# Performance work log

Measured on AMD Instinct MI355X. Metric: run time of the kernel, lower is better.

The kernel has to match this reference:

```python
import jax, jax.numpy as jnp
import numpy as np


def setup_inputs() -> dict:
    key = jax.random.key(0)
    k1, k2, k3, k4 = jax.random.split(key, 4)
    b, h, w = 16, 28, 28
    C = 3072  # 1024 + 2048
    L1 = 9    # num_landmarks + 1
    K = 2000  # num_classes
    l3 = jax.random.normal(k1, (b, 1024, h, w), dtype=jnp.float32)
    l4 = jax.random.normal(k2, (b, 2048, h // 2, w // 2), dtype=jnp.float32)
    W_land = jax.random.normal(k3, (L1, C), dtype=jnp.float32) * 0.02  # 1x1 conv weight
    W_class = jax.random.normal(k4, (K, C), dtype=jnp.float32) * 0.02
    modulation = jnp.ones((1, C, L1), dtype=jnp.float32)
    return {"l3": l3, "l4": l4, "W_land": W_land, "W_class": W_class, "modulation": modulation}


def reference(l3, l4, W_land, W_class, modulation):
    b, c3, h, w = l3.shape
    # bilinear upsample layer4 to layer3 spatial size (align_corners=False semantics)
    l4_up = jax.image.resize(l4, (l4.shape[0], l4.shape[1], h, w), method="bilinear")
    x = jnp.concatenate([l4_up, l3], axis=1)  # (b, 3072, h, w)

    ab = jnp.einsum("lc,bchw->blhw", W_land, x)            # (b, L+1, h, w)
    b_sq = jnp.sum(x * x, axis=1, keepdims=True)           # (b, 1, h, w)
    a_sq = jnp.sum(W_land * W_land, axis=1)[None, :, None, None]  # (1, L+1, 1, 1)
    maps = jax.nn.softmax(-(b_sq - 2.0 * ab + a_sq), axis=1)      # channel softmax (Softmax2d)

    # weighted spatial pooling: mean over h and w of maps[:,None]*x[:,:,None]
    hw = h * w
    all_features = jnp.einsum("blhw,bchw->bcl", maps, x) / hw     # (b, C, L+1)

    # modulation; dropout layers are identity at inference
    modulated = all_features * modulation                           # (b, C, L+1)
    scores = jnp.einsum("kc,bcl->bkl", W_class, modulated)          # (b, K, L+1)
    class_scores = jnp.mean(scores[:, :, :-1], axis=-1)             # (b, K)
    return class_scores, maps, all_features
```

## Files before the change

kernel.cpp:

```cpp
#include <hip/hip_runtime.h>
#include <math.h>

#define C_TOTAL 3072
#define C4 2048
#define C3 1024
#define HW  784
#define W_  28
#define HW4 196
#define W4  14
#define L_TOT 9
#define NB  16
#define NK  2000
#define J3  16

__device__ __forceinline__ void up_taps(int o, int& i0, int& i1, float& w0, float& w1) {
    int j = o >> 1;
    if (o & 1) { i0 = j;                       i1 = (j + 1 < W4) ? j + 1 : W4 - 1; w0 = 0.75f; w1 = 0.25f; }
    else       { i0 = (j - 1 > 0) ? j - 1 : 0; i1 = j;                             w0 = 0.25f; w1 = 0.75f; }
}

__device__ __forceinline__ float wdown(int o, int s) {
    int i0, i1; float w0, w1;
    up_taps(o, i0, i1, w0, w1);
    return (i0 == s ? w0 : 0.f) + (i1 == s ? w1 : 0.f);
}

__global__ __launch_bounds__(256) void abx_kernel(
    const float* __restrict__ l3, const float* __restrict__ l4,
    const float* __restrict__ Wl,
    float* __restrict__ ab4p, float* __restrict__ ab3p, float* __restrict__ asqp)
{
    const int bx = blockIdx.x;
    const int b  = blockIdx.y;
    const int tid = threadIdx.x;

    if (bx < 16) {
        const int q = tid;
        if (q >= HW4) return;
        const float* l4b = l4 + (size_t)b * C4 * HW4;
        float acc[L_TOT];
        #pragma unroll
        for (int l = 0; l < L_TOT; ++l) acc[l] = 0.f;
        const int c0 = bx * 128;
        #pragma unroll 8
        for (int i = 0; i < 128; ++i) {
            const int c = c0 + i;
            float xv = l4b[(size_t)c * HW4 + q];
            const float* wc = Wl + c;
            #pragma unroll
            for (int l = 0; l < L_TOT; ++l) acc[l] = fmaf(wc[l * C_TOTAL], xv, acc[l]);
        }
        float* outp = ab4p + (size_t)(bx * NB + b) * (L_TOT * HW4) + q;
        #pragma unroll
        for (int l = 0; l < L_TOT; ++l) outp[l * HW4] = acc[l];
    } else if (bx < 32) {
        const int t = tid;
        const int j = bx - 16;
        if (t >= HW / 4) return;
        const float4* l3b = (const float4*)(l3 + (size_t)b * C3 * HW);
        float4 acc[L_TOT];
        #pragma unroll
        for (int l = 0; l < L_TOT; ++l) acc[l] = make_float4(0.f, 0.f, 0.f, 0.f);
        const int c0 = j * (C3 / J3);
        #pragma unroll 8
        for (int i = 0; i < C3 / J3; ++i) {
            const int c = c0 + i;
            float4 xv = l3b[(size_t)c * (HW / 4) + t];
            const float* wc = Wl + C4 + c;
            #pragma unroll
            for (int l = 0; l < L_TOT; ++l) {
                const float w = wc[l * C_TOTAL];
                acc[l].x = fmaf(w, xv.x, acc[l].x);
                acc[l].y = fmaf(w, xv.y, acc[l].y);
                acc[l].z = fmaf(w, xv.z, acc[l].z);
                acc[l].w = fmaf(w, xv.w, acc[l].w);
            }
        }
        float4* outp = (float4*)(ab3p + (size_t)(j * NB + b) * (L_TOT * HW));
        #pragma unroll
        for (int l = 0; l < L_TOT; ++l) outp[l * (HW / 4) + t] = acc[l];
    } else {
        if (b != 0) return;
        __shared__ float red[4];
        for (int l = 0; l < L_TOT; ++l) {
            const float* wrow = Wl + (size_t)l * C_TOTAL;
            float s0 = 0.f, s1 = 0.f, s2 = 0.f, s3 = 0.f;
            {
                float a = wrow[tid +  0 * 256];
                float bb = wrow[tid + 1 * 256];
                float c = wrow[tid +  2 * 256];
                float d = wrow[tid +  3 * 256];
                float e = wrow[tid +  4 * 256];
                float f = wrow[tid +  5 * 256];
                float gg = wrow[tid + 6 * 256];
                float h = wrow[tid +  7 * 256];
                float i2 = wrow[tid + 8 * 256];
                float j2 = wrow[tid + 9 * 256];
                float k2 = wrow[tid + 10 * 256];
                float m2 = wrow[tid + 11 * 256];
                s0 = fmaf(a, a, fmaf(e, e, i2 * i2));
                s1 = fmaf(bb, bb, fmaf(f, f, j2 * j2));
                s2 = fmaf(c, c, fmaf(gg, gg, k2 * k2));
                s3 = fmaf(d, d, fmaf(h, h, m2 * m2));
            }
            float s = (s0 + s1) + (s2 + s3);
            #pragma unroll
            for (int off = 32; off; off >>= 1) s += __shfl_down(s, off, 64);
            const int w = tid >> 6, lane = tid & 63;
            if (lane == 0) red[w] = s;
            __syncthreads();
            if (tid == 0) asqp[l] = (red[0] + red[1]) + (red[2] + red[3]);
            __syncthreads();
        }
    }
}

__global__ __launch_bounds__(256) void maps_fin_kernel(
    const float* __restrict__ ab3p, const float* __restrict__ ab4p,
    const float* __restrict__ asqp, float* __restrict__ maps_out)
{
    __shared__ float ab4s[L_TOT * HW4];
    __shared__ float asq_s[L_TOT];

    const int tid = threadIdx.x;
    const int b   = blockIdx.y;
    const int p   = blockIdx.x * 256 + tid;

    for (int v = tid; v < L_TOT * HW4; v += 256) {
        float s = 0.f;
        #pragma unroll
        for (int j = 0; j < 16; ++j) s += ab4p[(size_t)(j * NB + b) * (L_TOT * HW4) + v];
        ab4s[v] = s;
    }
    if (tid < L_TOT) asq_s[tid] = asqp[tid];
    __syncthreads();
    if (p >= HW) return;

    const int y = p / W_, x = p % W_;
    int y0, y1, x0, x1; float wy0, wy1, wx0, wx1;
    up_taps(y, y0, y1, wy0, wy1);
    up_taps(x, x0, x1, wx0, wx1);

    float lg[L_TOT];
    #pragma unroll
    for (int l = 0; l < L_TOT; ++l) {
        float s = 0.f;
        #pragma unroll
        for (int j = 0; j < J3; ++j)
            s += ab3p[((size_t)(j * NB + b) * L_TOT + l) * HW + p];
        const float* a = ab4s + l * HW4;
        float t0 = fmaf(a[y0 * W4 + x1], wx1, a[y0 * W4 + x0] * wx0);
        float t1 = fmaf(a[y1 * W4 + x1], wx1, a[y1 * W4 + x0] * wx0);
        float up = fmaf(t1, wy1, t0 * wy0);
        lg[l] = 2.f * (s + up) - asq_s[l];
    }
    float m = lg[0];
    #pragma unroll
    for (int l = 1; l < L_TOT; ++l) m = fmaxf(m, lg[l]);
    float sum = 0.f;
    #pragma unroll
    for (int l = 0; l < L_TOT; ++l) { lg[l] = __expf(lg[l] - m); sum += lg[l]; }
    const float inv = 1.f / sum;
    float* mp = maps_out + (size_t)b * L_TOT * HW + p;
    #pragma unroll
    for (int l = 0; l < L_TOT; ++l) mp[l * HW] = lg[l] * inv;
}

__global__ __launch_bounds__(256) void pool_kernel(
    const float* __restrict__ l3, const float* __restrict__ l4,
    const float* __restrict__ maps, const float* __restrict__ modulation,
    float* __restrict__ af_out, float* __restrict__ g_out)
{
    __shared__ float msh[L_TOT * HW];

    const int tid  = threadIdx.x;
    const int b    = blockIdx.y;
    const int cblk = blockIdx.x;
    const bool isl4 = (cblk < 32);
    const float* mb = maps + (size_t)b * L_TOT * HW;

    if (isl4) {
        for (int v = tid; v < L_TOT * HW4; v += 256) {
            const int l = v / HW4, q = v % HW4;
            const int sy = q / W4, sx = q % W4;
            float s = 0.f;
            int oy0 = 2 * sy - 1; if (oy0 < 0) oy0 = 0;
            int oy1 = 2 * sy + 2; if (oy1 > 27) oy1 = 27;
            int ox0 = 2 * sx - 1; if (ox0 < 0) ox0 = 0;
            int ox1 = 2 * sx + 2; if (ox1 > 27) ox1 = 27;
            for (int oy = oy0; oy <= oy1; ++oy) {
                const float wy = wdown(oy, sy);
                const float* row = mb + l * HW + oy * W_;
                for (int ox = ox0; ox <= ox1; ++ox)
                    s = fmaf(wy * wdown(ox, sx), row[ox], s);
            }
            msh[v] = s;
        }
    } else {
        for (int v = tid; v < (L_TOT * HW) / 4; v += 256)
            ((float4*)msh)[v] = ((const float4*)mb)[v];
    }
    __syncthreads();

    const int   PMAX  = isl4 ? HW4 : HW;
    const float* xbase = isl4 ? (l4 + (size_t)b * C4 * HW4)
                              : (l3 + (size_t)b * C3 * HW);
    const int cloc0 = (isl4 ? cblk : (cblk - 32)) * 64;
    const int w = tid >> 6, s = (tid >> 4) & 3, t = tid & 15;
    const int cl = cloc0 + w * 16 + s * 4;

    float acc[4][L_TOT];
    #pragma unroll
    for (int j = 0; j < 4; ++j)
        #pragma unroll
        for (int l = 0; l < L_TOT; ++l) acc[j][l] = 0.f;

    const int kmax = isl4 ? 4 : 13;
    for (int k = 0; k < kmax; ++k) {
        const int p = (t << 2) + (k << 6);
        if (p < PMAX) {
            float4 m4[L_TOT];
            #pragma unroll
            for (int l = 0; l < L_TOT; ++l) m4[l] = *(const float4*)&msh[l * PMAX + p];
            #pragma unroll
            for (int j = 0; j < 4; ++j) {
                float4 x4 = *(const float4*)&xbase[(size_t)(cl + j) * PMAX + p];
                #pragma unroll
                for (int l = 0; l < L_TOT; ++l)
                    acc[j][l] = fmaf(x4.x, m4[l].x, fmaf(x4.y, m4[l].y,
                                fmaf(x4.z, m4[l].z, fmaf(x4.w, m4[l].w, acc[j][l]))));
            }
        }
    }

    #pragma unroll
    for (int j = 0; j < 4; ++j)
        #pragma unroll
        for (int l = 0; l < L_TOT; ++l) {
            float v = acc[j][l];
            v += __shfl_xor(v, 1, 16);
            v += __shfl_xor(v, 2, 16);
            v += __shfl_xor(v, 4, 16);
            v += __shfl_xor(v, 8, 16);
            acc[j][l] = v;
        }

    if (t == 0) {
        const float inv_hw = 1.f / 784.f;
        #pragma unroll
        for (int j = 0; j < 4; ++j) {
            const int cg = (isl4 ? 0 : C4) + cl + j;
            float* afp = af_out + ((size_t)b * C_TOTAL + cg) * L_TOT;
            float gp = 0.f;
            #pragma unroll
            for (int l = 0; l < L_TOT; ++l) {
                float v = acc[j][l] * inv_hw;
                afp[l] = v;
                if (l < 8) gp = fmaf(modulation[cg * L_TOT + l], v, gp);
            }
            g_out[(size_t)b * C_TOTAL + cg] = gp * 0.125f;
        }
    }
}

__global__ __launch_bounds__(256) void class_kernel(
    const float* __restrict__ Wc, const float* __restrict__ g,
    float* __restrict__ out)
{
    const int wv   = threadIdx.x >> 6;
    const int lane = threadIdx.x & 63;
    const int k    = blockIdx.x * 4 + wv;

    const float4* w4p = (const float4*)(Wc + (size_t)k * C_TOTAL);
    float acc[NB];
    #pragma unroll
    for (int b = 0; b < NB; ++b) acc[b] = 0.f;

    for (int i = 0; i < C_TOTAL / 256; ++i) {
        const int c4i = i * 64 + lane;
        float4 w4 = w4p[c4i];
        #pragma unroll
        for (int b = 0; b < NB; ++b) {
            float4 g4 = ((const float4*)(g + (size_t)b * C_TOTAL))[c4i];
            acc[b] = fmaf(w4.x, g4.x, acc[b]);
            acc[b] = fmaf(w4.y, g4.y, acc[b]);
            acc[b] = fmaf(w4.z, g4.z, acc[b]);
            acc[b] = fmaf(w4.w, g4.w, acc[b]);
        }
    }
    #pragma unroll
    for (int b = 0; b < NB; ++b) {
        #pragma unroll
        for (int off = 32; off; off >>= 1) acc[b] += __shfl_down(acc[b], off, 64);
    }
    if (lane == 0) {
        #pragma unroll
        for (int b = 0; b < NB; ++b) out[(size_t)b * NK + k] = acc[b];
    }
}

extern "C" void kernel_launch(void* const* d_in, const int* in_sizes, int n_in,
                              void* d_out, int out_size, void* d_ws, size_t ws_size,
                              hipStream_t stream) {
    const float* l3  = (const float*)d_in[0];
    const float* l4  = (const float*)d_in[1];
    const float* Wl  = (const float*)d_in[2];
    const float* Wc  = (const float*)d_in[3];
    const float* mod = (const float*)d_in[4];

    float* out  = (float*)d_out;
    float* cls  = out;
    float* maps = out + 32000;
    float* af   = out + 144896;

    float* ab4p = (float*)d_ws;
    float* ab3p = ab4p + 16 * NB * L_TOT * HW4;
    float* g    = ab3p + (size_t)J3 * NB * L_TOT * HW;
    float* asqp = g + NB * C_TOTAL;

    abx_kernel     <<<dim3(33, NB), 256, 0, stream>>>(l3, l4, Wl, ab4p, ab3p, asqp);
    maps_fin_kernel<<<dim3(4, NB), 256, 0, stream>>>(ab3p, ab4p, asqp, maps);
    pool_kernel    <<<dim3(48, NB), 256, 0, stream>>>(l3, l4, maps, mod, af, g);
    class_kernel   <<<NK / 4, 256, 0, stream>>>(Wc, g, cls);
}
```

Before: 189.5 us.

## Accumulate landmark dot products atomically and precompute downsampled maps once per batch

The abx kernel now adds its per-chunk partial products into a single zeroed buffer with atomicAdd, replacing the 16-way partial buffers that maps_fin then summed. That cuts workspace traffic and the reduction reads, at the cost of a memset and contended float atomics whose summation order is nondeterministic. The bilinear downsample of the maps, which every layer4 pool block recomputed, now runs once per batch in a new small kernel, trading that redundant work for an extra launch.

```diff
diff --git a/kernel.cpp b/kernel.cpp
--- a/kernel.cpp
+++ b/kernel.cpp
@@ -28,7 +28,7 @@
 __global__ __launch_bounds__(256) void abx_kernel(
     const float* __restrict__ l3, const float* __restrict__ l4,
     const float* __restrict__ Wl,
-    float* __restrict__ ab4p, float* __restrict__ ab3p, float* __restrict__ asqp)
+    float* __restrict__ ab4sum, float* __restrict__ absum, float* __restrict__ asqp)
 {
     const int bx = blockIdx.x;
     const int b  = blockIdx.y;
@@ -50,9 +50,9 @@
             #pragma unroll
             for (int l = 0; l < L_TOT; ++l) acc[l] = fmaf(wc[l * C_TOTAL], xv, acc[l]);
         }
-        float* outp = ab4p + (size_t)(bx * NB + b) * (L_TOT * HW4) + q;
-        #pragma unroll
-        for (int l = 0; l < L_TOT; ++l) outp[l * HW4] = acc[l];
+        float* outp = ab4sum + (size_t)b * (L_TOT * HW4) + q;
+        #pragma unroll
+        for (int l = 0; l < L_TOT; ++l) atomicAdd(&outp[l * HW4], acc[l]);
     } else if (bx < 32) {
         const int t = tid;
         const int j = bx - 16;
@@ -76,9 +76,15 @@
                 acc[l].w = fmaf(w, xv.w, acc[l].w);
             }
         }
-        float4* outp = (float4*)(ab3p + (size_t)(j * NB + b) * (L_TOT * HW));
-        #pragma unroll
-        for (int l = 0; l < L_TOT; ++l) outp[l * (HW / 4) + t] = acc[l];
+        float* outp = absum + (size_t)b * (L_TOT * HW) + t * 4;
+        #pragma unroll
+        for (int l = 0; l < L_TOT; ++l) {
+            float* o = outp + l * HW;
+            atomicAdd(&o[0], acc[l].x);
+            atomicAdd(&o[1], acc[l].y);
+            atomicAdd(&o[2], acc[l].z);
+            atomicAdd(&o[3], acc[l].w);
+        }
     } else {
         if (b != 0) return;
         __shared__ float red[4];
@@ -116,7 +122,7 @@
 }
 
 __global__ __launch_bounds__(256) void maps_fin_kernel(
-    const float* __restrict__ ab3p, const float* __restrict__ ab4p,
+    const float* __restrict__ absum, const float* __restrict__ ab4sum,
     const float* __restrict__ asqp, float* __restrict__ maps_out)
 {
     __shared__ float ab4s[L_TOT * HW4];
@@ -126,12 +132,8 @@
     const int b   = blockIdx.y;
     const int p   = blockIdx.x * 256 + tid;
 
-    for (int v = tid; v < L_TOT * HW4; v += 256) {
-        float s = 0.f;
-        #pragma unroll
-        for (int j = 0; j < 16; ++j) s += ab4p[(size_t)(j * NB + b) * (L_TOT * HW4) + v];
-        ab4s[v] = s;
-    }
+    for (int v = tid; v < L_TOT * HW4; v += 256)
+        ab4s[v] = ab4sum[(size_t)b * (L_TOT * HW4) + v];
     if (tid < L_TOT) asq_s[tid] = asqp[tid];
     __syncthreads();
     if (p >= HW) return;
@@ -141,13 +143,11 @@
     up_taps(y, y0, y1, wy0, wy1);
     up_taps(x, x0, x1, wx0, wx1);
 
+    const float* ap = absum + (size_t)b * (L_TOT * HW) + p;
     float lg[L_TOT];
     #pragma unroll
     for (int l = 0; l < L_TOT; ++l) {
-        float s = 0.f;
-        #pragma unroll
-        for (int j = 0; j < J3; ++j)
-            s += ab3p[((size_t)(j * NB + b) * L_TOT + l) * HW + p];
+        float s = ap[l * HW];
         const float* a = ab4s + l * HW4;
         float t0 = fmaf(a[y0 * W4 + x1], wx1, a[y0 * W4 + x0] * wx0);
         float t1 = fmaf(a[y1 * W4 + x1], wx1, a[y1 * W4 + x0] * wx0);
@@ -166,9 +166,34 @@
     for (int l = 0; l < L_TOT; ++l) mp[l * HW] = lg[l] * inv;
 }
 
+__global__ __launch_bounds__(256) void mapsdown_kernel(
+    const float* __restrict__ maps, float* __restrict__ mdown)
+{
+    const int b   = blockIdx.x;
+    const int tid = threadIdx.x;
+    const float* mb = maps + (size_t)b * L_TOT * HW;
+    for (int v = tid; v < L_TOT * HW4; v += 256) {
+        const int l = v / HW4, q = v % HW4;
+        const int sy = q / W4, sx = q % W4;
+        float s = 0.f;
+        int oy0 = 2 * sy - 1; if (oy0 < 0) oy0 = 0;
+        int oy1 = 2 * sy + 2; if (oy1 > 27) oy1 = 27;
+        int ox0 = 2 * sx - 1; if (ox0 < 0) ox0 = 0;
+        int ox1 = 2 * sx + 2; if (ox1 > 27) ox1 = 27;
+        for (int oy = oy0; oy <= oy1; ++oy) {
+            const float wy = wdown(oy, sy);
+            const float* row = mb + l * HW + oy * W_;
+            for (int ox = ox0; ox <= ox1; ++ox)
+                s = fmaf(wy * wdown(ox, sx), row[ox], s);
+        }
+        mdown[(size_t)b * (L_TOT * HW4) + v] = s;
+    }
+}
+
 __global__ __launch_bounds__(256) void pool_kernel(
     const float* __restrict__ l3, const float* __restrict__ l4,
-    const float* __restrict__ maps, const float* __restrict__ modulation,
+    const float* __restrict__ maps, const float* __restrict__ mdown,
+    const float* __restrict__ modulation,
     float* __restrict__ af_out, float* __restrict__ g_out)
 {
     __shared__ float msh[L_TOT * HW];
@@ -177,28 +202,15 @@
     const int b    = blockIdx.y;
     const int cblk = blockIdx.x;
     const bool isl4 = (cblk < 32);
-    const float* mb = maps + (size_t)b * L_TOT * HW;
 
     if (isl4) {
-        for (int v = tid; v < L_TOT * HW4; v += 256) {
-            const int l = v / HW4, q = v % HW4;
-            const int sy = q / W4, sx = q % W4;
-            float s = 0.f;
-            int oy0 = 2 * sy - 1; if (oy0 < 0) oy0 = 0;
-            int oy1 = 2 * sy + 2; if (oy1 > 27) oy1 = 27;
-            int ox0 = 2 * sx - 1; if (ox0 < 0) ox0 = 0;
-            int ox1 = 2 * sx + 2; if (ox1 > 27) ox1 = 27;
-            for (int oy = oy0; oy <= oy1; ++oy) {
-                const float wy = wdown(oy, sy);
-                const float* row = mb + l * HW + oy * W_;
-                for (int ox = ox0; ox <= ox1; ++ox)
-                    s = fmaf(wy * wdown(ox, sx), row[ox], s);
-            }
-            msh[v] = s;
-        }
+        const float4* src = (const float4*)(mdown + (size_t)b * (L_TOT * HW4));
+        for (int v = tid; v < (L_TOT * HW4) / 4; v += 256)
+            ((float4*)msh)[v] = src[v];
     } else {
+        const float4* src = (const float4*)(maps + (size_t)b * L_TOT * HW);
         for (int v = tid; v < (L_TOT * HW) / 4; v += 256)
-            ((float4*)msh)[v] = ((const float4*)mb)[v];
+            ((float4*)msh)[v] = src[v];
     }
     __syncthreads();
 
@@ -313,13 +325,17 @@
     float* maps = out + 32000;
     float* af   = out + 144896;
 
-    float* ab4p = (float*)d_ws;
-    float* ab3p = ab4p + 16 * NB * L_TOT * HW4;
-    float* g    = ab3p + (size_t)J3 * NB * L_TOT * HW;
-    float* asqp = g + NB * C_TOTAL;
-
-    abx_kernel     <<<dim3(33, NB), 256, 0, stream>>>(l3, l4, Wl, ab4p, ab3p, asqp);
-    maps_fin_kernel<<<dim3(4, NB), 256, 0, stream>>>(ab3p, ab4p, asqp, maps);
-    pool_kernel    <<<dim3(48, NB), 256, 0, stream>>>(l3, l4, maps, mod, af, g);
+    float* absum  = (float*)d_ws;
+    float* ab4sum = absum + NB * L_TOT * HW;
+    float* asqp   = ab4sum + NB * L_TOT * HW4;
+    float* mdown  = asqp + 16;
+    float* g      = mdown + NB * L_TOT * HW4;
+
+    hipMemsetAsync(absum, 0, (size_t)(NB * L_TOT * HW + NB * L_TOT * HW4) * sizeof(float), stream);
+
+    abx_kernel     <<<dim3(33, NB), 256, 0, stream>>>(l3, l4, Wl, ab4sum, absum, asqp);
+    maps_fin_kernel<<<dim3(4, NB), 256, 0, stream>>>(absum, ab4sum, asqp, maps);
+    mapsdown_kernel<<<NB, 256, 0, stream>>>(maps, mdown);
+    pool_kernel    <<<dim3(48, NB), 256, 0, stream>>>(l3, l4, maps, mdown, mod, af, g);
     class_kernel   <<<NK / 4, 256, 0, stream>>>(Wc, g, cls);
 }
```

After: 211.6 us. 11.7% more time.
